# Kernel optimization log

Hardware: AMD Instinct MI355X
Metric: run time of the kernel (lower is better)

The kernel has to match this reference:

```python
import jax, jax.numpy as jnp
import numpy as np

EPS = 1e-12

def _l2norm(v):
    # torch.nn.functional.normalize(p=2) with eps clamp
    return v / jnp.maximum(jnp.linalg.norm(v), EPS)

def _spectral_weight(W, U):
    # W: (out, in) flattened 1x1 conv weight; U: (1, out) power-iteration buffer.
    # One power iteration, all under stop_gradient (torch.no_grad in original).
    V = _l2norm(U @ W)            # (1, in)
    Unew = _l2norm(V @ W.T)       # (1, out)
    sigma = (Unew @ W @ V.T)[0, 0]
    return W / jax.lax.stop_gradient(sigma)

def _conv1x1(x, W, b):
    # x: (b,c,h,w), W: (o,c), b: (o,)
    return jnp.einsum('oc,bchw->bohw', W, x) + b[None, :, None, None]

def setup_inputs() -> dict:
    key = jax.random.key(0)
    ks = jax.random.split(key, 11)
    B, C, H, W = 4, 256, 64, 64
    Ck = C // 8
    return {
        'x':   jax.random.normal(ks[0], (B, C, H, W), jnp.float32),
        'f_w': jax.random.normal(ks[1], (Ck, C), jnp.float32) * 0.05,
        'f_b': jax.random.normal(ks[2], (Ck,), jnp.float32) * 0.05,
        'f_u': jax.random.uniform(ks[3], (1, Ck), jnp.float32),
        'g_w': jax.random.normal(ks[4], (Ck, C), jnp.float32) * 0.05,
        'g_b': jax.random.normal(ks[5], (Ck,), jnp.float32) * 0.05,
        'g_u': jax.random.uniform(ks[6], (1, Ck), jnp.float32),
        'h_w': jax.random.normal(ks[7], (C, C), jnp.float32) * 0.05,
        'h_b': jax.random.normal(ks[8], (C,), jnp.float32) * 0.05,
        'h_u': jax.random.uniform(ks[9], (1, C), jnp.float32),
        'gamma': jax.random.normal(ks[10], (1, 1), jnp.float32),
    }

def reference(x, f_w, f_b, f_u, g_w, g_b, g_u, h_w, h_b, h_u, gamma):
    b, c, h, w = x.shape
    hw = h * w
    key_ = _conv1x1(x, _spectral_weight(f_w, f_u), f_b).reshape(b, -1, hw).transpose(0, 2, 1)  # (b,hw,ck)
    query = _conv1x1(x, _spectral_weight(g_w, g_u), g_b).reshape(b, -1, hw)                    # (b,ck,hw)
    attn = jax.nn.softmax(jnp.einsum('bnd,bdm->bnm', key_, query), axis=-1)                    # (b,hw,hw)
    value = _conv1x1(x, _spectral_weight(h_w, h_u), h_b).reshape(b, -1, hw)                    # (b,c,hw)
    out = jnp.einsum('bnm,bcm->bnc', attn, value)                                              # (b,hw,c)
    # Faithful to original: raw view of (b,hw,c) contiguous buffer into (b,c,h,w)
    out = out.reshape(b, c, h, w)
    return gamma[0, 0] * out + x
```

## Files before the change

kernel.cpp:

```cpp
#include <hip/hip_runtime.h>


constexpr int kC   = 256;
constexpr int kHW  = 4096;
constexpr int kB   = 4;
constexpr int kCHW = kC * kHW;

typedef short bf16x8 __attribute__((ext_vector_type(8)));
typedef float f32x4  __attribute__((ext_vector_type(4)));
typedef unsigned short u16;

#if __has_builtin(__builtin_amdgcn_exp2f)
#define EXP2(x) __builtin_amdgcn_exp2f(x)
#else
#define EXP2(x) exp2f(x)
#endif

__device__ __forceinline__ u16 f2bf(float f) {
    union { float f; unsigned u; } v; v.f = f;
    unsigned u = v.u;
    return (u16)((u + 0x7fffu + ((u >> 16) & 1u)) >> 16);
}
__device__ __forceinline__ float bf2f(u16 h) {
    union { unsigned u; float f; } v; v.u = ((unsigned)h) << 16;
    return v.f;
}

__global__ __launch_bounds__(1024) void k_pack(
    const float* __restrict__ fw, const float* __restrict__ gw,
    const float* __restrict__ hww,
    u16* __restrict__ wh, u16* __restrict__ wl)
{
    const int tid = blockIdx.x * 1024 + threadIdx.x;
    const int g  = tid >> 8;
    const int ci = tid & 255;
    const float f = (g < 32) ? fw[g * 256 + ci]
                  : (g < 64) ? gw[(g - 32) * 256 + ci]
                             : hww[(g - 64) * 256 + ci];
    const int idx = ((g >> 4) * 8 + (ci >> 5)) * 512 + (g & 15) * 32 + (ci & 31);
    const u16 h = f2bf(f);
    wh[idx] = h;
    wl[idx] = f2bf(f - bf2f(h));
}

__global__ __launch_bounds__(1024) void k_sigma(
    const float* __restrict__ fw, const float* __restrict__ fu,
    const float* __restrict__ gw, const float* __restrict__ gu,
    const float* __restrict__ hww, const float* __restrict__ hu,
    float* __restrict__ sig)
{
    const int which = blockIdx.x;
    const float* W = which == 0 ? fw : (which == 1 ? gw : hww);
    const float* U = which == 0 ? fu : (which == 1 ? gu : hu);
    const int O = (which == 2) ? 256 : 32;
    const int t = threadIdx.x;

    __shared__ float par[4][256];
    __shared__ float red[256];
    __shared__ __align__(16) float Vv[256];

    {
        const int i = t & 255, och = t >> 8;
        float p = 0.f;
        if (O == 256) {
            const float* Wc = W + (size_t)(och * 64) * 256 + i;
            const float* Uc = U + och * 64;
#pragma unroll 8
            for (int oo = 0; oo < 64; ++oo)
                p += Uc[oo] * Wc[(size_t)oo * 256];
        } else if (och == 0) {
            const float* Wc = W + i;
#pragma unroll 8
            for (int oo = 0; oo < 32; ++oo)
                p += U[oo] * Wc[(size_t)oo * 256];
        }
        par[och][i] = p;
    }
    __syncthreads();
    float t1 = 0.f;
    if (t < 256) {
        t1 = par[0][t] + par[1][t] + par[2][t] + par[3][t];
        red[t] = t1 * t1;
    }
    __syncthreads();
    for (int s = 128; s > 0; s >>= 1) { if (t < s) red[t] += red[t + s]; __syncthreads(); }
    if (t < 256) Vv[t] = t1 / fmaxf(sqrtf(red[0]), 1e-12f);
    __syncthreads();

    {
        const int o = t & 255, ich = t >> 8;
        float q = 0.f;
        if (o < O) {
            const float4* Wr = (const float4*)(W + (size_t)o * 256 + ich * 64);
            const float4* Vr = (const float4*)(&Vv[ich * 64]);
#pragma unroll
            for (int j = 0; j < 16; ++j) {
                const float4 w = Wr[j]; const float4 v = Vr[j];
                q += w.x * v.x + w.y * v.y + w.z * v.z + w.w * v.w;
            }
        }
        par[ich][o] = q;
    }
    __syncthreads();
    if (t < 256) {
        const float t2 = par[0][t] + par[1][t] + par[2][t] + par[3][t];
        red[t] = t2 * t2;
    }
    __syncthreads();
    for (int s = 128; s > 0; s >>= 1) { if (t < s) red[t] += red[t + s]; __syncthreads(); }
    if (t == 0) {
        const float s2 = red[0];
        sig[which] = fmaxf(sqrtf(s2), 1e-12f) / s2;
    }
}

__global__ __launch_bounds__(512) void k_proj(
    const float* __restrict__ x,
    const u16* __restrict__ wh, const u16* __restrict__ wl,
    const float* __restrict__ fb, const float* __restrict__ gb,
    const float* __restrict__ hb, const float* __restrict__ sig,
    u16* __restrict__ Kc, u16* __restrict__ Qc, u16* __restrict__ Vb)
{
    __shared__ __align__(16) float xs[256][64];
    __shared__ float bLDS[320];

    const int t = threadIdx.x;
    const int wave = t >> 6, lane = t & 63;
    const int quad = lane >> 4, l15 = lane & 15;
    const int b = blockIdx.y;
    const int n0 = blockIdx.x * 64;
    const int nch = wave & 3, cohalf = wave >> 2;

    constexpr float kLog2e = 1.44269504f;

    {
        const int r4i = lane >> 4, c16 = lane & 15;
        const float* xg = x + (size_t)b * kCHW + (size_t)r4i * kHW + n0 + c16 * 4;
#pragma unroll
        for (int j = 0; j < 8; ++j) {
            const int cibase = (wave * 8 + j) * 4;
            __builtin_amdgcn_global_load_lds(
                (const __attribute__((address_space(1))) void*)(xg + (size_t)cibase * kHW),
                (__attribute__((address_space(3))) void*)&xs[cibase][0], 16, 0, 0);
        }
    }
    if (t < 320) bLDS[t] = (t < 32) ? fb[t]
                         : (t < 64) ? gb[t - 32] * kLog2e
                         : hb[t - 64];
    __syncthreads();

    const int n = nch * 16 + l15;
    bf16x8 bh[8], bl[8];
#pragma unroll
    for (int s = 0; s < 8; ++s) {
        union { u16 a[8]; bf16x8 v; } H, L;
#pragma unroll
        for (int j = 0; j < 8; ++j) {
            const float v = xs[s * 32 + quad * 8 + j][n];
            const u16 h = f2bf(v);
            H.a[j] = h; L.a[j] = f2bf(v - bf2f(h));
        }
        bh[s] = H.v; bl[s] = L.v;
    }

    const u16* whp = wh + l15 * 32 + quad * 8;
    const u16* wlp = wl + l15 * 32 + quad * 8;

    f32x4 acc[10] = {};
#pragma unroll
    for (int c = 0; c < 10; ++c) {
        const size_t base = (size_t)(cohalf * 10 + c) * 4096;
#pragma unroll
        for (int s = 0; s < 8; ++s) {
            const bf16x8 ah = *(const bf16x8*)(whp + base + s * 512);
            const bf16x8 al = *(const bf16x8*)(wlp + base + s * 512);
            acc[c] = __builtin_amdgcn_mfma_f32_16x16x32_bf16(ah, bh[s], acc[c], 0, 0, 0);
            acc[c] = __builtin_amdgcn_mfma_f32_16x16x32_bf16(ah, bl[s], acc[c], 0, 0, 0);
            acc[c] = __builtin_amdgcn_mfma_f32_16x16x32_bf16(al, bh[s], acc[c], 0, 0, 0);
        }
    }

    const float s0 = sig[0], s1 = sig[1] * kLog2e, s2 = sig[2];
#pragma unroll
    for (int c = 0; c < 10; ++c) {
        const int cog0 = (cohalf * 10 + c) * 16;
        const float inv = (cog0 < 32) ? s0 : (cog0 < 64) ? s1 : s2;
        if (cog0 < 64) {
            u16 hi[4], lo[4];
#pragma unroll
            for (int r = 0; r < 4; ++r) {
                const float v = acc[c][r] * inv + bLDS[cog0 + quad * 4 + r];
                hi[r] = f2bf(v);
                lo[r] = f2bf(v - bf2f(hi[r]));
            }
            u16* H = (cog0 < 32) ? Kc : Qc;
            const int dbase = (cog0 & 31) + quad * 4;
            const size_t off = (size_t)(b * kHW + n0 + n) * 64;
            const unsigned h01 = (unsigned)hi[0] | ((unsigned)hi[1] << 16);
            const unsigned h23 = (unsigned)hi[2] | ((unsigned)hi[3] << 16);
            const unsigned l01 = (unsigned)lo[0] | ((unsigned)lo[1] << 16);
            const unsigned l23 = (unsigned)lo[2] | ((unsigned)lo[3] << 16);
            *(uint2*)(H + off + dbase)      = make_uint2(h01, h23);
            *(uint2*)(H + off + 32 + dbase) = make_uint2(l01, l23);
        } else {
#pragma unroll
            for (int r = 0; r < 4; ++r) {
                const int co = cog0 + quad * 4 + r;
                const float v = acc[c][r] * inv + bLDS[co];
                Vb[((size_t)b * kC + (co - 64)) * kHW + n0 + n] = f2bf(v);
            }
        }
    }
}

__global__ __launch_bounds__(512, 4) void k_attn(
    const u16* __restrict__ Kc, const u16* __restrict__ Qc,
    const u16* __restrict__ Vb,
    u16* __restrict__ Op, float* __restrict__ Sl)
{
    __shared__ __align__(16) u16 Qt[2][4096];
    __shared__ __align__(16) u16 Pt[2][4096];
    __shared__ float lsum[8][16];

    const int t = threadIdx.x;
    const int wave = t >> 6, lane = t & 63;
    const int quad = lane >> 4, l15 = lane & 15;
    const int sg = wave >> 1, half = wave & 1;

    const int id = blockIdx.x;
    const int xcd = id & 7;
    const int b = xcd >> 1;
    const int nb0 = ((xcd & 1) * 32 + ((id >> 3) & 31)) * 64;
    const int mh = id >> 8;
    const int mt0 = mh * 32, mt1 = mt0 + 32;

    const u16* Kb  = Kc + (size_t)b * kHW * 64;
    const u16* Qb  = Qc + (size_t)b * kHW * 64;
    const u16* Vbb = Vb + (size_t)b * kC * kHW;

    const size_t krow = (size_t)(nb0 + sg * 16 + l15) * 64 + (size_t)quad * 8;
    const bf16x8 kh = *(const bf16x8*)(Kb + krow);
    const bf16x8 kl = *(const bf16x8*)(Kb + krow + 32);

    const u16* vrow[2];
#pragma unroll
    for (int ct = 0; ct < 2; ++ct)
        vrow[ct] = Vbb + (size_t)(wave * 32 + ct * 16 + l15) * kHW + quad * 8;

    const int qs_row = lane >> 3, qs_ch = lane & 7;
    const int rloc = wave * 8 + qs_row;
    const int qswz = (qs_ch ^ (rloc & 7)) << 3;

    f32x4 O[8] = {};
    float lrow = 0.f;
    bf16x8 vc[4];

    __builtin_amdgcn_global_load_lds(
        (const __attribute__((address_space(1))) void*)
            (Qb + (size_t)(mt0 * 64 + rloc) * 64 + qswz),
        (__attribute__((address_space(3))) void*)&Qt[0][wave * 512], 16, 0, 0);
    __syncthreads();

    for (int mt = mt0; mt < mt1; ++mt) {
        const int cur = mt & 1;
        const int m0 = mt * 64;

        if (mt < mt1 - 1) {
            __builtin_amdgcn_global_load_lds(
                (const __attribute__((address_space(1))) void*)
                    (Qb + (size_t)(m0 + 64 + rloc) * 64 + qswz),
                (__attribute__((address_space(3))) void*)&Qt[cur ^ 1][wave * 512], 16, 0, 0);
        }
#pragma unroll
        for (int ct = 0; ct < 2; ++ct)
#pragma unroll
            for (int ks = 0; ks < 2; ++ks)
                vc[ct * 2 + ks] = *(const bf16x8*)(vrow[ct] + m0 + ks * 32);

        f32x4 s[2];
        __builtin_amdgcn_s_setprio(1);
#pragma unroll
        for (int mi2 = 0; mi2 < 2; ++mi2) {
            const int mi = half * 2 + mi2;
            const int rbase = (mi * 16 + l15) * 64;
            const bf16x8 qhv = *(const bf16x8*)&Qt[cur][rbase + ((quad       ^ (l15 & 7)) << 3)];
            const bf16x8 qlv = *(const bf16x8*)&Qt[cur][rbase + (((quad + 4) ^ (l15 & 7)) << 3)];
            f32x4 a = { 0.f, 0.f, 0.f, 0.f };
            a = __builtin_amdgcn_mfma_f32_16x16x32_bf16(qhv, kl, a, 0, 0, 0);
            a = __builtin_amdgcn_mfma_f32_16x16x32_bf16(qlv, kh, a, 0, 0, 0);
            a = __builtin_amdgcn_mfma_f32_16x16x32_bf16(qhv, kh, a, 0, 0, 0);
            s[mi2] = a;
        }
        __builtin_amdgcn_s_setprio(0);

        {
            const int prow = sg * 16 + l15;
#pragma unroll
            for (int mi2 = 0; mi2 < 2; ++mi2) {
                const float p0 = EXP2(s[mi2][0]);
                const float p1 = EXP2(s[mi2][1]);
                const float p2 = EXP2(s[mi2][2]);
                const float p3 = EXP2(s[mi2][3]);
                lrow += (p0 + p1) + (p2 + p3);
                const unsigned d0 = __builtin_amdgcn_perm(
                    __float_as_uint(p1), __float_as_uint(p0), 0x07060302u);
                const unsigned d1 = __builtin_amdgcn_perm(
                    __float_as_uint(p3), __float_as_uint(p2), 0x07060302u);
                const int mi = half * 2 + mi2;
                const int chunk = 2 * mi + (quad >> 1);
                const int off = prow * 64 + ((chunk ^ (l15 & 7)) << 3) + (quad & 1) * 4;
                *(uint2*)(Pt[cur] + off) = make_uint2(d0, d1);
            }
        }

        __syncthreads();

        __builtin_amdgcn_s_setprio(1);
#pragma unroll
        for (int ks = 0; ks < 2; ++ks) {
#pragma unroll
            for (int rg = 0; rg < 4; ++rg) {
                const bf16x8 pa = *(const bf16x8*)&Pt[cur][(rg * 16 + l15) * 64
                                     + (((ks * 4 + quad) ^ (l15 & 7)) << 3)];
#pragma unroll
                for (int ct = 0; ct < 2; ++ct)
                    O[rg * 2 + ct] = __builtin_amdgcn_mfma_f32_16x16x32_bf16(
                        pa, vc[ct * 2 + ks], O[rg * 2 + ct], 0, 0, 0);
            }
        }
        __builtin_amdgcn_s_setprio(0);
    }

    lrow += __shfl_xor(lrow, 16);
    lrow += __shfl_xor(lrow, 32);
    if (lane < 16) lsum[wave][l15] = lrow;
    __syncthreads();
    if (half == 0 && lane < 16)
        Sl[(size_t)(mh * 4 + b) * kHW + nb0 + sg * 16 + l15]
            = lsum[wave][l15] + lsum[wave ^ 1][l15];

    u16* Opb = Op + (size_t)(mh * 4 + b) * kHW * 256;
#pragma unroll
    for (int rg = 0; rg < 4; ++rg) {
#pragma unroll
        for (int ct = 0; ct < 2; ++ct) {
#pragma unroll
            for (int r = 0; r < 4; ++r) {
                const int nn = nb0 + rg * 16 + quad * 4 + r;
                const int c = wave * 32 + ct * 16 + l15;
                Opb[(size_t)nn * 256 + c] = f2bf(O[rg * 2 + ct][r]);
            }
        }
    }
}

__global__ __launch_bounds__(256) void k_merge(
    const float* __restrict__ x, const float* __restrict__ gamma,
    const u16* __restrict__ Op, const float* __restrict__ Sl,
    float* __restrict__ out)
{
    const int tid = blockIdx.x * 256 + threadIdx.x;
    const int cg = tid & 31;
    const int n  = (tid >> 5) & 4095;
    const int b  = tid >> 17;
    const int c0 = cg * 8;

    const float la = Sl[(size_t)b * kHW + n];
    const float lb = Sl[(size_t)(4 + b) * kHW + n];
    const float invL = 1.f / (la + lb);
    const float g = gamma[0];

    const size_t base = ((size_t)b * kHW + n) * 256 + c0;
    const uint4 A = *(const uint4*)(Op + base);
    const uint4 B = *(const uint4*)(Op + base + (size_t)4 * kHW * 256);
    const float4 x0 = *(const float4*)(x + base);
    const float4 x1 = *(const float4*)(x + base + 4);

    float o[8];
    const unsigned aw[4] = { A.x, A.y, A.z, A.w };
    const unsigned bw[4] = { B.x, B.y, B.z, B.w };
#pragma unroll
    for (int j = 0; j < 8; ++j) {
        const float va = bf2f((u16)(aw[j >> 1] >> ((j & 1) * 16)));
        const float vb = bf2f((u16)(bw[j >> 1] >> ((j & 1) * 16)));
        o[j] = (va + vb) * invL;
    }
    float4 r0, r1;
    r0.x = g * o[0] + x0.x; r0.y = g * o[1] + x0.y;
    r0.z = g * o[2] + x0.z; r0.w = g * o[3] + x0.w;
    r1.x = g * o[4] + x1.x; r1.y = g * o[5] + x1.y;
    r1.z = g * o[6] + x1.z; r1.w = g * o[7] + x1.w;
    *(float4*)(out + base)     = r0;
    *(float4*)(out + base + 4) = r1;
}

extern "C" void kernel_launch(void* const* d_in, const int* in_sizes, int n_in,
                              void* d_out, int out_size, void* d_ws, size_t ws_size,
                              hipStream_t stream)
{
    const float* x     = (const float*)d_in[0];
    const float* fw    = (const float*)d_in[1];
    const float* fb    = (const float*)d_in[2];
    const float* fu    = (const float*)d_in[3];
    const float* gw    = (const float*)d_in[4];
    const float* gb    = (const float*)d_in[5];
    const float* gu    = (const float*)d_in[6];
    const float* hww   = (const float*)d_in[7];
    const float* hb    = (const float*)d_in[8];
    const float* hu    = (const float*)d_in[9];
    const float* gamma = (const float*)d_in[10];
    float* out = (float*)d_out;

    char* ws = (char*)d_ws;
    float* sig = (float*)ws;
    u16* wh = (u16*)(ws + 1024);
    u16* wl = wh + 320 * 256;
    u16* Kc = (u16*)(ws + (1u << 20));
    u16* Qc = (u16*)(ws + (3u << 20));
    u16* Vb = (u16*)(ws + (5u << 20));
    u16* Op = (u16*)(ws + (16u << 20));
    float* Sl = (float*)(ws + (32u << 20));

    k_pack<<<dim3(80), dim3(1024), 0, stream>>>(fw, gw, hww, wh, wl);
    k_sigma<<<dim3(3), dim3(1024), 0, stream>>>(fw, fu, gw, gu, hww, hu, sig);
    k_proj<<<dim3(64, 4), dim3(512), 0, stream>>>(x, wh, wl, fb, gb, hb, sig,
                                                  Kc, Qc, Vb);
    k_attn<<<dim3(512), dim3(512), 0, stream>>>(Kc, Qc, Vb, Op, Sl);
    k_merge<<<dim3(2048), dim3(256), 0, stream>>>(x, gamma, Op, Sl, out);
}
```

Before: 220.3 us.

## Software-pipeline QK and PV stages in attention, merge pack and sigma kernels

The attention loop is restructured so each iteration computes QK scores and exp/pack for tile mt while running the P·V MFMAs for tile mt-1. A third P buffer in LDS allows this with one barrier per iteration, and V registers are double-buffered (vc/vn). This aims to overlap exp and LDS-write latency with matrix work. The weight-pack and spectral-sigma kernels are merged into one launch to save a kernel launch. The cost is more LDS and register pressure, which may hurt occupancy at 4 blocks per CU.

Result: no change. 218.0 us (-1.1%).

```diff
diff --git a/kernel.cpp b/kernel.cpp
--- a/kernel.cpp
+++ b/kernel.cpp
@@ -26,29 +26,26 @@
     return v.f;
 }
 
-__global__ __launch_bounds__(1024) void k_pack(
-    const float* __restrict__ fw, const float* __restrict__ gw,
-    const float* __restrict__ hww,
-    u16* __restrict__ wh, u16* __restrict__ wl)
-{
-    const int tid = blockIdx.x * 1024 + threadIdx.x;
-    const int g  = tid >> 8;
-    const int ci = tid & 255;
-    const float f = (g < 32) ? fw[g * 256 + ci]
-                  : (g < 64) ? gw[(g - 32) * 256 + ci]
-                             : hww[(g - 64) * 256 + ci];
-    const int idx = ((g >> 4) * 8 + (ci >> 5)) * 512 + (g & 15) * 32 + (ci & 31);
-    const u16 h = f2bf(f);
-    wh[idx] = h;
-    wl[idx] = f2bf(f - bf2f(h));
-}
-
-__global__ __launch_bounds__(1024) void k_sigma(
+__global__ __launch_bounds__(1024) void k_prep(
     const float* __restrict__ fw, const float* __restrict__ fu,
     const float* __restrict__ gw, const float* __restrict__ gu,
     const float* __restrict__ hww, const float* __restrict__ hu,
-    float* __restrict__ sig)
+    float* __restrict__ sig, u16* __restrict__ wh, u16* __restrict__ wl)
 {
+    if (blockIdx.x >= 3) {
+        const int tid = (blockIdx.x - 3) * 1024 + threadIdx.x;
+        const int g  = tid >> 8;
+        const int ci = tid & 255;
+        const float f = (g < 32) ? fw[g * 256 + ci]
+                      : (g < 64) ? gw[(g - 32) * 256 + ci]
+                                 : hww[(g - 64) * 256 + ci];
+        const int idx = ((g >> 4) * 8 + (ci >> 5)) * 512 + (g & 15) * 32 + (ci & 31);
+        const u16 h = f2bf(f);
+        wh[idx] = h;
+        wl[idx] = f2bf(f - bf2f(h));
+        return;
+    }
+
     const int which = blockIdx.x;
     const float* W = which == 0 ? fw : (which == 1 ? gw : hww);
     const float* U = which == 0 ? fu : (which == 1 ? gu : hu);
@@ -219,7 +216,7 @@
     u16* __restrict__ Op, float* __restrict__ Sl)
 {
     __shared__ __align__(16) u16 Qt[2][4096];
-    __shared__ __align__(16) u16 Pt[2][4096];
+    __shared__ __align__(16) u16 Pt[3][4096];
     __shared__ float lsum[8][16];
 
     const int t = threadIdx.x;
@@ -253,7 +250,64 @@
 
     f32x4 O[8] = {};
     float lrow = 0.f;
-    bf16x8 vc[4];
+    bf16x8 vc[4], vn[4];
+
+#define QK_TILE(buf, sdst)                                                        \
+    {                                                                             \
+        __builtin_amdgcn_s_setprio(1);                                            \
+        _Pragma("unroll")                                                         \
+        for (int mi2 = 0; mi2 < 2; ++mi2) {                                       \
+            const int mi = half * 2 + mi2;                                        \
+            const int rbase = (mi * 16 + l15) * 64;                               \
+            const bf16x8 qhv = *(const bf16x8*)&Qt[buf][rbase + ((quad       ^ (l15 & 7)) << 3)]; \
+            const bf16x8 qlv = *(const bf16x8*)&Qt[buf][rbase + (((quad + 4) ^ (l15 & 7)) << 3)]; \
+            f32x4 a = { 0.f, 0.f, 0.f, 0.f };                                     \
+            a = __builtin_amdgcn_mfma_f32_16x16x32_bf16(qhv, kl, a, 0, 0, 0);     \
+            a = __builtin_amdgcn_mfma_f32_16x16x32_bf16(qlv, kh, a, 0, 0, 0);     \
+            a = __builtin_amdgcn_mfma_f32_16x16x32_bf16(qhv, kh, a, 0, 0, 0);     \
+            sdst[mi2] = a;                                                        \
+        }                                                                         \
+        __builtin_amdgcn_s_setprio(0);                                            \
+    }
+
+#define PACK_TILE(pi, ssrc)                                                       \
+    {                                                                             \
+        const int prow = sg * 16 + l15;                                           \
+        _Pragma("unroll")                                                         \
+        for (int mi2 = 0; mi2 < 2; ++mi2) {                                       \
+            const float p0 = EXP2(ssrc[mi2][0]);                                  \
+            const float p1 = EXP2(ssrc[mi2][1]);                                  \
+            const float p2 = EXP2(ssrc[mi2][2]);                                  \
+            const float p3 = EXP2(ssrc[mi2][3]);                                  \
+            lrow += (p0 + p1) + (p2 + p3);                                        \
+            const unsigned d0 = __builtin_amdgcn_perm(                            \
+                __float_as_uint(p1), __float_as_uint(p0), 0x07060302u);           \
+            const unsigned d1 = __builtin_amdgcn_perm(                            \
+                __float_as_uint(p3), __float_as_uint(p2), 0x07060302u);           \
+            const int mi = half * 2 + mi2;                                        \
+            const int chunk = 2 * mi + (quad >> 1);                               \
+            const int off = prow * 64 + ((chunk ^ (l15 & 7)) << 3) + (quad & 1) * 4; \
+            *(uint2*)(Pt[pi] + off) = make_uint2(d0, d1);                         \
+        }                                                                         \
+    }
+
+#define PV_TILE(pi, vsrc)                                                         \
+    {                                                                             \
+        __builtin_amdgcn_s_setprio(1);                                            \
+        _Pragma("unroll")                                                         \
+        for (int ks = 0; ks < 2; ++ks) {                                          \
+            _Pragma("unroll")                                                     \
+            for (int rg = 0; rg < 4; ++rg) {                                      \
+                const bf16x8 pa = *(const bf16x8*)&Pt[pi][(rg * 16 + l15) * 64    \
+                                     + (((ks * 4 + quad) ^ (l15 & 7)) << 3)];     \
+                _Pragma("unroll")                                                 \
+                for (int ct = 0; ct < 2; ++ct)                                    \
+                    O[rg * 2 + ct] = __builtin_amdgcn_mfma_f32_16x16x32_bf16(     \
+                        pa, vsrc[ct * 2 + ks], O[rg * 2 + ct], 0, 0, 0);          \
+            }                                                                     \
+        }                                                                         \
+        __builtin_amdgcn_s_setprio(0);                                            \
+    }
 
     __builtin_amdgcn_global_load_lds(
         (const __attribute__((address_space(1))) void*)
@@ -261,8 +315,26 @@
         (__attribute__((address_space(3))) void*)&Qt[0][wave * 512], 16, 0, 0);
     __syncthreads();
 
-    for (int mt = mt0; mt < mt1; ++mt) {
+    {
+        __builtin_amdgcn_global_load_lds(
+            (const __attribute__((address_space(1))) void*)
+                (Qb + (size_t)((mt0 + 1) * 64 + rloc) * 64 + qswz),
+            (__attribute__((address_space(3))) void*)&Qt[1][wave * 512], 16, 0, 0);
+#pragma unroll
+        for (int ct = 0; ct < 2; ++ct)
+#pragma unroll
+            for (int ks = 0; ks < 2; ++ks)
+                vc[ct * 2 + ks] = *(const bf16x8*)(vrow[ct] + mt0 * 64 + ks * 32);
+        f32x4 s[2];
+        QK_TILE(0, s);
+        PACK_TILE(mt0 % 3, s);
+        __syncthreads();
+    }
+
+    for (int mt = mt0 + 1; mt < mt1; ++mt) {
         const int cur = mt & 1;
+        const int pi = mt % 3;
+        const int pprev = (mt + 2) % 3;
         const int m0 = mt * 64;
 
         if (mt < mt1 - 1) {
@@ -275,61 +347,24 @@
         for (int ct = 0; ct < 2; ++ct)
 #pragma unroll
             for (int ks = 0; ks < 2; ++ks)
-                vc[ct * 2 + ks] = *(const bf16x8*)(vrow[ct] + m0 + ks * 32);
+                vn[ct * 2 + ks] = *(const bf16x8*)(vrow[ct] + m0 + ks * 32);
 
         f32x4 s[2];
-        __builtin_amdgcn_s_setprio(1);
-#pragma unroll
-        for (int mi2 = 0; mi2 < 2; ++mi2) {
-            const int mi = half * 2 + mi2;
-            const int rbase = (mi * 16 + l15) * 64;
-            const bf16x8 qhv = *(const bf16x8*)&Qt[cur][rbase + ((quad       ^ (l15 & 7)) << 3)];
-            const bf16x8 qlv = *(const bf16x8*)&Qt[cur][rbase + (((quad + 4) ^ (l15 & 7)) << 3)];
-            f32x4 a = { 0.f, 0.f, 0.f, 0.f };
-            a = __builtin_amdgcn_mfma_f32_16x16x32_bf16(qhv, kl, a, 0, 0, 0);
-            a = __builtin_amdgcn_mfma_f32_16x16x32_bf16(qlv, kh, a, 0, 0, 0);
-            a = __builtin_amdgcn_mfma_f32_16x16x32_bf16(qhv, kh, a, 0, 0, 0);
-            s[mi2] = a;
-        }
-        __builtin_amdgcn_s_setprio(0);
-
-        {
-            const int prow = sg * 16 + l15;
-#pragma unroll
-            for (int mi2 = 0; mi2 < 2; ++mi2) {
-                const float p0 = EXP2(s[mi2][0]);
-                const float p1 = EXP2(s[mi2][1]);
-                const float p2 = EXP2(s[mi2][2]);
-                const float p3 = EXP2(s[mi2][3]);
-                lrow += (p0 + p1) + (p2 + p3);
-                const unsigned d0 = __builtin_amdgcn_perm(
-                    __float_as_uint(p1), __float_as_uint(p0), 0x07060302u);
-                const unsigned d1 = __builtin_amdgcn_perm(
-                    __float_as_uint(p3), __float_as_uint(p2), 0x07060302u);
-                const int mi = half * 2 + mi2;
-                const int chunk = 2 * mi + (quad >> 1);
-                const int off = prow * 64 + ((chunk ^ (l15 & 7)) << 3) + (quad & 1) * 4;
-                *(uint2*)(Pt[cur] + off) = make_uint2(d0, d1);
-            }
-        }
+        QK_TILE(cur, s);
+        PACK_TILE(pi, s);
+        PV_TILE(pprev, vc);
 
         __syncthreads();
 
-        __builtin_amdgcn_s_setprio(1);
-#pragma unroll
-        for (int ks = 0; ks < 2; ++ks) {
-#pragma unroll
-            for (int rg = 0; rg < 4; ++rg) {
-                const bf16x8 pa = *(const bf16x8*)&Pt[cur][(rg * 16 + l15) * 64
-                                     + (((ks * 4 + quad) ^ (l15 & 7)) << 3)];
-#pragma unroll
-                for (int ct = 0; ct < 2; ++ct)
-                    O[rg * 2 + ct] = __builtin_amdgcn_mfma_f32_16x16x32_bf16(
-                        pa, vc[ct * 2 + ks], O[rg * 2 + ct], 0, 0, 0);
-            }
-        }
-        __builtin_amdgcn_s_setprio(0);
-    }
+#pragma unroll
+        for (int i = 0; i < 4; ++i) vc[i] = vn[i];
+    }
+
+    PV_TILE((mt1 - 1) % 3, vc);
+
+#undef QK_TILE
+#undef PACK_TILE
+#undef PV_TILE
 
     lrow += __shfl_xor(lrow, 16);
     lrow += __shfl_xor(lrow, 32);
@@ -421,8 +456,7 @@
     u16* Op = (u16*)(ws + (16u << 20));
     float* Sl = (float*)(ws + (32u << 20));
 
-    k_pack<<<dim3(80), dim3(1024), 0, stream>>>(fw, gw, hww, wh, wl);
-    k_sigma<<<dim3(3), dim3(1024), 0, stream>>>(fw, fu, gw, gu, hww, hu, sig);
+    k_prep<<<dim3(83), dim3(1024), 0, stream>>>(fw, fu, gw, gu, hww, hu, sig, wh, wl);
     k_proj<<<dim3(64, 4), dim3(512), 0, stream>>>(x, wh, wl, fb, gb, hb, sig,
                                                   Kc, Qc, Vb);
     k_attn<<<dim3(512), dim3(512), 0, stream>>>(Kc, Qc, Vb, Op, Sl);
```
